# Kernel optimization log

Hardware: AMD Instinct MI355X
Metric: run time of the kernel (lower is better)

Reference implementation:

```python
import jax, jax.numpy as jnp
import numpy as np

B, S, DIN, DIM, H = 2, 2304, 1024, 1024, 16
HEAD_DIM = DIM // H            # 64
ROT_DIM = HEAD_DIM             # partial_rotary_factor = 1
BASE = 10000.0
EPS = 1e-6


def setup_inputs() -> dict:
    key = jax.random.key(0)
    ks = jax.random.split(key, 6)
    return {
        "input": jax.random.normal(ks[0], (B, S, DIN), dtype=jnp.float32),
        "qkv_w": jax.random.normal(ks[1], (3 * DIM, DIN), dtype=jnp.float32) * 0.02,
        "qkv_b": jnp.zeros((3 * DIM,), dtype=jnp.float32),
        "q_scale": jnp.ones((DIM,), dtype=jnp.float32),
        "k_scale": jnp.ones((DIM,), dtype=jnp.float32),
        "proj_w": jax.random.normal(ks[2], (DIN, DIM), dtype=jnp.float32) * 0.02,
        "proj_b": jnp.zeros((DIN,), dtype=jnp.float32),
        "height": 48,
        "width": 48,
    }


def _rms_norm(x, scale):
    # RMSNorm over the full inner dim (QKNorm), learned scale
    var = jnp.mean(x * x, axis=-1, keepdims=True)
    return x * jax.lax.rsqrt(var + EPS) * scale


def _rope_1d(x, pos):
    # x: (b, n, h, d_ax), pos: (n,) float; rotate_half-style RoPE
    d = x.shape[-1]
    inv_freq = 1.0 / (BASE ** (jnp.arange(0, d, 2, dtype=jnp.float32) / d))  # (d/2,)
    ang = pos[:, None] * inv_freq                                            # (n, d/2)
    cos = jnp.concatenate([jnp.cos(ang), jnp.cos(ang)], axis=-1)[None, :, None, :]
    sin = jnp.concatenate([jnp.sin(ang), jnp.sin(ang)], axis=-1)[None, :, None, :]
    x1, x2 = jnp.split(x, 2, axis=-1)
    rot = jnp.concatenate([-x2, x1], axis=-1)
    return x * cos + rot * sin


def _rope_2d(x, height, width):
    # axial 2D RoPE: first half of rotary dims keyed by row, second half by col
    n = height * width
    idx = jnp.arange(n, dtype=jnp.float32)
    rows = jnp.floor(idx / width)
    cols = jnp.mod(idx, width)
    half = ROT_DIM // 2
    x_r = _rope_1d(x[..., :half], rows)
    x_c = _rope_1d(x[..., half:ROT_DIM], cols)
    return jnp.concatenate([x_r, x_c, x[..., ROT_DIM:]], axis=-1)


def reference(input, qkv_w, qkv_b, q_scale, k_scale, proj_w, proj_b, height, width):
    b, n, _ = input.shape
    qkv = input @ qkv_w.T + qkv_b                       # (b, n, 3*dim)
    q, k, v = jnp.split(qkv, 3, axis=-1)
    q = _rms_norm(q, q_scale)
    k = _rms_norm(k, k_scale)
    # (b, n, h, d)
    q = q.reshape(b, n, H, HEAD_DIM)
    k = k.reshape(b, n, H, HEAD_DIM)
    v = v.reshape(b, n, H, HEAD_DIM)
    q = _rope_2d(q, height, width)
    k = _rope_2d(k, height, width)
    scale = HEAD_DIM ** (-0.5)
    # (b, h, q, k)
    scores = jnp.einsum("bqhd,bkhd->bhqk", q, k) * scale
    attn = jax.nn.softmax(scores, axis=-1)
    out = jnp.einsum("bhqk,bkhd->bqhd", attn, v)        # (b, n, h, d)
    out = out.reshape(b, n, DIM)
    return out @ proj_w.T + proj_b
```

## Files before the change

### kernel.cpp

```cpp
#include <hip/hip_runtime.h>
#include <math.h>

#define BB   2
#define SS   2304
#define DINC 1024
#define DIMC 1024
#define HH   16
#define HD   64

typedef _Float16 half_t;
typedef __attribute__((ext_vector_type(4))) _Float16 half4;
typedef __attribute__((ext_vector_type(8))) _Float16 half8;
typedef __attribute__((ext_vector_type(4))) float    f32x4;

#define LOG2E 1.44269504088896340736f
#define EXP2(x) __builtin_amdgcn_exp2f(x)

#define GLOAD_LDS16(gp, lp)                                                     \
    __builtin_amdgcn_global_load_lds(                                           \
        (const __attribute__((address_space(1))) void*)(gp),                    \
        (__attribute__((address_space(3))) void*)(lp), 16, 0, 0)

template<int RB>
__global__ __launch_bounds__(256)
void convert_tile_f16(const float* __restrict__ src, half_t* __restrict__ dst, int K)
{
    constexpr int EPT = RB * 32 / 256;
    const int mb = blockIdx.x;
    const int kb = blockIdx.y;
    const int t  = threadIdx.x;
    const int e0 = t * EPT;
    const int mm = e0 >> 5;
    const int kk = e0 & 31;
    const float* sp = src + (size_t)(mb * RB + mm) * K + kb * 32 + kk;
    half_t*      dp = dst + ((size_t)mb * (K >> 5) + kb) * (RB * 32) + mm * 32 + kk;
    #pragma unroll
    for (int g = 0; g < EPT / 4; ++g) {
        float4 v = *(const float4*)(sp + 4 * g);
        dp[4 * g + 0] = (half_t)v.x; dp[4 * g + 1] = (half_t)v.y;
        dp[4 * g + 2] = (half_t)v.z; dp[4 * g + 3] = (half_t)v.w;
    }
}

template<int BN, bool OUT_HALF>
__global__ __launch_bounds__(256)
void gemm_mfma(const half_t* __restrict__ Ah, const half_t* __restrict__ Bh,
               const float* __restrict__ bias, void* __restrict__ Cout,
               int M, int N, int K)
{
    constexpr int MT = (BN == 128) ? 4 : 2;
    constexpr int NT = 4;
    const int KB = K >> 5;
    __shared__ half_t As[8192];
    __shared__ half_t Bs[2 * BN * 32];

    const int t    = threadIdx.x;
    const int w    = t >> 6;
    const int lane = t & 63;
    const int l15  = lane & 15, quad = lane >> 4;
    const int wr   = (BN == 128) ? (w >> 1) : w;
    const int wc   = (BN == 128) ? (w & 1) : 0;
    const int mb   = blockIdx.y, nb = blockIdx.x;

    f32x4 acc[MT][NT];
    #pragma unroll
    for (int mt = 0; mt < MT; ++mt)
        #pragma unroll
        for (int nt = 0; nt < NT; ++nt) acc[mt][nt] = (f32x4){0.f, 0.f, 0.f, 0.f};

    const half_t* atile = Ah + (size_t)mb * KB * 4096;
    const half_t* btile = Bh + (size_t)nb * KB * (BN * 32);

    for (int kb = 0; kb < KB; kb += 2) {
        #pragma unroll
        for (int u = 0; u < 2; ++u) {
            const half_t* at = atile + (size_t)(kb + u) * 4096;
            const half_t* bt = btile + (size_t)(kb + u) * (BN * 32);
            #pragma unroll
            for (int v = 0; v < 2; ++v) {
                const int ch = w * 2 + v;
                GLOAD_LDS16(at + ch * 512 + lane * 8, As + u * 4096 + ch * 512);
            }
            if (BN == 128) {
                #pragma unroll
                for (int v = 0; v < 2; ++v) {
                    const int ch = w * 2 + v;
                    GLOAD_LDS16(bt + ch * 512 + lane * 8, Bs + u * 4096 + ch * 512);
                }
            } else {
                GLOAD_LDS16(bt + w * 512 + lane * 8, Bs + u * (BN * 32) + w * 512);
            }
        }
        __syncthreads();

        #pragma unroll
        for (int u = 0; u < 2; ++u) {
            half8 af[MT], bf[NT];
            #pragma unroll
            for (int mt = 0; mt < MT; ++mt)
                af[mt] = *(const half8*)(As + u * 4096
                                         + (wr * (MT * 16) + mt * 16 + l15) * 32 + quad * 8);
            #pragma unroll
            for (int nt = 0; nt < NT; ++nt)
                bf[nt] = *(const half8*)(Bs + u * (BN * 32)
                                         + (wc * 64 + nt * 16 + l15) * 32 + quad * 8);
            #pragma unroll
            for (int mt = 0; mt < MT; ++mt)
                #pragma unroll
                for (int nt = 0; nt < NT; ++nt)
                    acc[mt][nt] = __builtin_amdgcn_mfma_f32_16x16x32_f16(
                        af[mt], bf[nt], acc[mt][nt], 0, 0, 0);
        }
        __syncthreads();
    }

    const int bm = mb * 128, bn = nb * BN;
    #pragma unroll
    for (int nt = 0; nt < NT; ++nt) {
        const int n  = bn + wc * 64 + nt * 16 + l15;
        const float bv = bias[n];
        #pragma unroll
        for (int mt = 0; mt < MT; ++mt) {
            const int m0 = bm + wr * (MT * 16) + mt * 16 + quad * 4;
            #pragma unroll
            for (int rg = 0; rg < 4; ++rg) {
                const float v = acc[mt][nt][rg] + bv;
                if (OUT_HALF) ((half_t*)Cout)[(size_t)(m0 + rg) * N + n] = (half_t)v;
                else          ((float*) Cout)[(size_t)(m0 + rg) * N + n] = v;
            }
        }
    }
}

__global__ __launch_bounds__(256)
void normrope_v7(half_t* __restrict__ qkvh, const float* __restrict__ q_scale,
                 const float* __restrict__ k_scale, const int* __restrict__ wptr,
                 half_t* __restrict__ Kf, half_t* __restrict__ Vf)
{
    const int token = blockIdx.x;
    const int s     = token % SS;
    const int b     = token / SS;
    const int w     = *wptr;
    const int t     = threadIdx.x;
    const float rowp = (float)(s / w);
    const float colp = (float)(s % w);

    half_t* base = qkvh + (size_t)token * 3072;

    const int c    = s >> 5;
    const int slot = s & 31;
    const int ktile = (slot >> 2) & 1;
    const int krow  = ((slot >> 3) << 2) + (slot & 3);

    {
        half4 v4 = *(const half4*)(base + 2048 + 4 * t);
        const int dabs0 = 4 * t;
        const int h  = dabs0 >> 6;
        const int sl3 = slot >> 3, sl7 = slot & 7;
        half_t* vdst = Vf + ((size_t)(b * HH + h) * 72 + c) * 2048;
        #pragma unroll
        for (int ii = 0; ii < 4; ++ii) {
            const int d = (dabs0 + ii) & 63;
            vdst[(d >> 4) * 512 + (sl3 * 16 + (d & 15)) * 8 + sl7] = v4[ii];
        }
    }

    __shared__ float buf[DIMC];
    __shared__ float red[4];

    #pragma unroll
    for (int sel = 0; sel < 2; ++sel) {
        half_t* row = base + sel * DIMC;
        const float* scp = sel ? k_scale : q_scale;

        half4 xh = *(const half4*)(row + 4 * t);
        float x0 = (float)xh[0], x1 = (float)xh[1], x2 = (float)xh[2], x3 = (float)xh[3];
        float ss = x0 * x0 + x1 * x1 + x2 * x2 + x3 * x3;
        #pragma unroll
        for (int o = 32; o >= 1; o >>= 1) ss += __shfl_xor(ss, o);
        if ((t & 63) == 0) red[t >> 6] = ss;
        __syncthreads();

        const float rinv = rsqrtf((red[0] + red[1] + red[2] + red[3]) * (1.0f / DIMC) + 1e-6f);
        float4 g = *(const float4*)(scp + 4 * t);
        buf[4 * t + 0] = x0 * rinv * g.x;
        buf[4 * t + 1] = x1 * rinv * g.y;
        buf[4 * t + 2] = x2 * rinv * g.z;
        buf[4 * t + 3] = x3 * rinv * g.w;
        __syncthreads();

        const float qsc = sel ? 1.0f : (0.125f * LOG2E);

        #pragma unroll
        for (int pp = 0; pp < 2; ++pp) {
            const int p = t + pp * 256;
            const int h = p >> 5;
            const int r = p & 31;
            const int j = r & 15;
            const float pos = (r < 16) ? rowp : colp;
            const int d1 = (r < 16) ? j : (32 + j);
            const int d2 = d1 + 16;
            const float freq = exp2f((float)j * -0.83048202372f);
            const float ang  = pos * freq;
            float sn, cs;
            __sincosf(ang, &sn, &cs);
            const float a1 = buf[h * HD + d1], a2 = buf[h * HD + d2];
            const float o1 = (a1 * cs - a2 * sn) * qsc;
            const float o2 = (a2 * cs + a1 * sn) * qsc;
            if (sel == 0) {
                row[h * HD + d1] = (half_t)o1;
                row[h * HD + d2] = (half_t)o2;
            } else {
                half_t* kdst = Kf + ((size_t)(b * HH + h) * 72 + c) * 2048;
                kdst[((ktile << 1) + (d1 >> 5)) * 512
                     + ((((d1 & 31) >> 3) << 4) + krow) * 8 + (d1 & 7)] = (half_t)o1;
                kdst[((ktile << 1) + (d2 >> 5)) * 512
                     + ((((d2 & 31) >> 3) << 4) + krow) * 8 + (d2 & 7)] = (half_t)o2;
            }
        }
        __syncthreads();
    }
}

__global__ __launch_bounds__(256, 3)
void flash_attn_mfma16(const half_t* __restrict__ qkvh, const half_t* __restrict__ Kf,
                       const half_t* __restrict__ Vf, half_t* __restrict__ attn_h)
{
    const int flat = blockIdx.x;
    const int xcd  = flat & 7;
    const int idx  = flat >> 3;
    const int bh   = xcd * 4 + idx / 24;
    const int qtb  = idx % 24;
    const int b    = bh >> 4, h = bh & 15;
    const int t    = threadIdx.x;
    const int w    = t >> 6;
    const int qh   = w >> 1;
    const int jt   = w & 1;
    const int lane = t & 63;
    const int l15  = lane & 15, quad = lane >> 4;

    const size_t tb = (size_t)b * SS;
    const int q0 = qtb * 96;

    __shared__ float mlb[4][48];
    __shared__ float Ob[2][64][49];

    half8 qf[3][2];
    #pragma unroll
    for (int qt = 0; qt < 3; ++qt)
        #pragma unroll
        for (int dg = 0; dg < 2; ++dg)
            qf[qt][dg] = *(const half8*)(qkvh + (tb + q0 + qh * 48 + qt * 16 + l15) * 3072
                                          + h * HD + dg * 32 + quad * 8);

    f32x4 acc[4][3];
    float lacc[3] = {0.f, 0.f, 0.f};
    #pragma unroll
    for (int qt = 0; qt < 3; ++qt)
        #pragma unroll
        for (int dt = 0; dt < 4; ++dt) acc[dt][qt] = (f32x4){0.f, 0.f, 0.f, 0.f};

    const half_t* kpl = Kf + (size_t)bh * 147456 + jt * 2048 + lane * 8;
    const half_t* vpl = Vf + (size_t)bh * 147456 + jt * 2048 + lane * 8;

    half8 k00 = *(const half8*)(kpl);
    half8 k01 = *(const half8*)(kpl + 512);
    half8 k10 = *(const half8*)(kpl + 1024);
    half8 k11 = *(const half8*)(kpl + 1536);
    half8 v0  = *(const half8*)(vpl);
    half8 v1  = *(const half8*)(vpl + 512);
    half8 v2  = *(const half8*)(vpl + 1024);
    half8 v3  = *(const half8*)(vpl + 1536);

    const f32x4 initC = (f32x4){-4.f, -4.f, -4.f, -4.f};

    for (int p = 0; p < 36; ++p) {
        f32x4 scA[3], scB[3];
        __builtin_amdgcn_s_setprio(1);
        #pragma unroll
        for (int qt = 0; qt < 3; ++qt) {
            scA[qt] = initC;
            scA[qt] = __builtin_amdgcn_mfma_f32_16x16x32_f16(k00, qf[qt][0], scA[qt], 0, 0, 0);
            scA[qt] = __builtin_amdgcn_mfma_f32_16x16x32_f16(k01, qf[qt][1], scA[qt], 0, 0, 0);
            scB[qt] = initC;
            scB[qt] = __builtin_amdgcn_mfma_f32_16x16x32_f16(k10, qf[qt][0], scB[qt], 0, 0, 0);
            scB[qt] = __builtin_amdgcn_mfma_f32_16x16x32_f16(k11, qf[qt][1], scB[qt], 0, 0, 0);
        }
        __builtin_amdgcn_s_setprio(0);

        if (p + 1 < 36) {
            const half_t* kN = kpl + (size_t)(p + 1) * 4096;
            k00 = *(const half8*)(kN);
            k01 = *(const half8*)(kN + 512);
            k10 = *(const half8*)(kN + 1024);
            k11 = *(const half8*)(kN + 1536);
        }

        half8 pf[3];
        #pragma unroll
        for (int qt = 0; qt < 3; ++qt) {
            const float a0 = EXP2(scA[qt][0]);
            const float a1 = EXP2(scA[qt][1]);
            const float a2 = EXP2(scA[qt][2]);
            const float a3 = EXP2(scA[qt][3]);
            const float b0 = EXP2(scB[qt][0]);
            const float b1 = EXP2(scB[qt][1]);
            const float b2 = EXP2(scB[qt][2]);
            const float b3 = EXP2(scB[qt][3]);
            lacc[qt] += ((a0 + a1) + (a2 + a3)) + ((b0 + b1) + (b2 + b3));
            pf[qt] = (half8){(half_t)a0, (half_t)a1, (half_t)a2, (half_t)a3,
                             (half_t)b0, (half_t)b1, (half_t)b2, (half_t)b3};
        }

        __builtin_amdgcn_s_setprio(1);
        #pragma unroll
        for (int dt = 0; dt < 4; ++dt) {
            const half8 vf = (dt == 0) ? v0 : (dt == 1) ? v1 : (dt == 2) ? v2 : v3;
            #pragma unroll
            for (int qt = 0; qt < 3; ++qt)
                acc[dt][qt] = __builtin_amdgcn_mfma_f32_16x16x32_f16(
                    vf, pf[qt], acc[dt][qt], 0, 0, 0);
        }
        __builtin_amdgcn_s_setprio(0);

        if (p + 1 < 36) {
            const half_t* vN = vpl + (size_t)(p + 1) * 4096;
            v0 = *(const half8*)(vN);
            v1 = *(const half8*)(vN + 512);
            v2 = *(const half8*)(vN + 1024);
            v3 = *(const half8*)(vN + 1536);
        }
    }

    #pragma unroll
    for (int qt = 0; qt < 3; ++qt) {
        float lq = lacc[qt];
        lq += __shfl_xor(lq, 16);
        lq += __shfl_xor(lq, 32);
        if (quad == 0) mlb[w][qt * 16 + l15] = lq;
    }
    __syncthreads();

    float fac[3];
    #pragma unroll
    for (int qt = 0; qt < 3; ++qt) {
        const int q = qt * 16 + l15;
        fac[qt] = 1.0f / (mlb[qh * 2 + 0][q] + mlb[qh * 2 + 1][q]);
    }

    #pragma unroll
    for (int ph = 0; ph < 2; ++ph) {
        if (jt == ph) {
            #pragma unroll
            for (int dt = 0; dt < 4; ++dt)
                #pragma unroll
                for (int qt = 0; qt < 3; ++qt)
                    #pragma unroll
                    for (int rg = 0; rg < 4; ++rg) {
                        const int d = dt * 16 + quad * 4 + rg;
                        const int q = qt * 16 + l15;
                        const float v = acc[dt][qt][rg] * fac[qt];
                        if (ph == 0) Ob[qh][d][q] = v;
                        else         Ob[qh][d][q] += v;
                    }
        }
        __syncthreads();
    }

    #pragma unroll
    for (int g2 = 0; g2 < 3; ++g2) {
        const int q  = g2 * 32 + (t >> 3);
        const int ds = (t & 7) * 8;
        const int qh2 = (q >= 48) ? 1 : 0;
        const int qq  = q - 48 * qh2;
        const size_t mrow = tb + q0 + q;
        const int mb2 = (int)(mrow >> 7);
        const int mm  = (int)(mrow & 127);
        const int kb2 = (h * HD + ds) >> 5;
        const int kk  = ds & 31;
        half8 o;
        #pragma unroll
        for (int ii = 0; ii < 8; ++ii) o[ii] = (half_t)Ob[qh2][ds + ii][qq];
        *(half8*)(attn_h + ((size_t)mb2 * 32 + kb2) * 4096 + mm * 32 + kk) = o;
    }
}

extern "C" void kernel_launch(void* const* d_in, const int* in_sizes, int n_in,
                              void* d_out, int out_size, void* d_ws, size_t ws_size,
                              hipStream_t stream)
{
    const float* input   = (const float*)d_in[0];
    const float* qkv_w   = (const float*)d_in[1];
    const float* qkv_b   = (const float*)d_in[2];
    const float* q_scale = (const float*)d_in[3];
    const float* k_scale = (const float*)d_in[4];
    const float* proj_w  = (const float*)d_in[5];
    const float* proj_b  = (const float*)d_in[6];
    const int*   width   = (const int*)d_in[8];
    float* out = (float*)d_out;

    half_t* qkvh   = (half_t*)d_ws;
    half_t* attn_h = qkvh   + (size_t)4608 * 3072;
    half_t* Vf     = attn_h + (size_t)4608 * 1024;
    half_t* Ah     = Vf     + (size_t)32 * 72 * 2048;
    half_t* Bh1    = Ah     + (size_t)4608 * 1024;
    half_t* Bh2    = Bh1    + (size_t)3072 * 1024;
    half_t* Kf     = Ah;

    const int M = BB * SS;

    convert_tile_f16<128><<<dim3(M / 128, DINC / 32),        256, 0, stream>>>(input,  Ah,  DINC);
    convert_tile_f16<128><<<dim3(3 * DIMC / 128, DINC / 32), 256, 0, stream>>>(qkv_w, Bh1, DINC);
    convert_tile_f16<64><<<dim3(DINC / 64, DIMC / 32),       256, 0, stream>>>(proj_w, Bh2, DIMC);

    gemm_mfma<128, true><<<dim3(3 * DIMC / 128, M / 128), 256, 0, stream>>>(
        Ah, Bh1, qkv_b, qkvh, M, 3 * DIMC, DINC);

    normrope_v7<<<M, 256, 0, stream>>>(qkvh, q_scale, k_scale, width, Kf, Vf);

    flash_attn_mfma16<<<dim3(768), 256, 0, stream>>>(qkvh, Kf, Vf, attn_h);

    gemm_mfma<64, false><<<dim3(DINC / 64, M / 128), 256, 0, stream>>>(
        attn_h, Bh2, proj_b, out, M, DINC, DIMC);
}
```

Baseline: 240.3 us.

## Use 192x96 tiles for the QKV GEMM so the grid fills one occupancy wave

Adds a dedicated QKV projection GEMM kernel with 192x96 block tiles and a 6x3 MFMA fragment grid per wave. The grid becomes 768 blocks, which with a minimum of 3 blocks per CU fits the device in one wave. It also changes the fp32-to-fp16 tile conversion so consecutive threads read consecutive float4s, for better coalescing, and matches its tiling to the new A and B tile shapes. The trade-off is higher register pressure from 18 accumulators per wave, and the new tile is specialised to fixed sizes.

Result: faster. 231.0 us (-3.9%).

```diff
diff --git a/kernel.cpp b/kernel.cpp
--- a/kernel.cpp
+++ b/kernel.cpp
@@ -25,20 +25,91 @@
 __global__ __launch_bounds__(256)
 void convert_tile_f16(const float* __restrict__ src, half_t* __restrict__ dst, int K)
 {
-    constexpr int EPT = RB * 32 / 256;
+    constexpr int NG = RB * 32 / 1024;
     const int mb = blockIdx.x;
     const int kb = blockIdx.y;
     const int t  = threadIdx.x;
-    const int e0 = t * EPT;
-    const int mm = e0 >> 5;
-    const int kk = e0 & 31;
-    const float* sp = src + (size_t)(mb * RB + mm) * K + kb * 32 + kk;
-    half_t*      dp = dst + ((size_t)mb * (K >> 5) + kb) * (RB * 32) + mm * 32 + kk;
-    #pragma unroll
-    for (int g = 0; g < EPT / 4; ++g) {
-        float4 v = *(const float4*)(sp + 4 * g);
-        dp[4 * g + 0] = (half_t)v.x; dp[4 * g + 1] = (half_t)v.y;
-        dp[4 * g + 2] = (half_t)v.z; dp[4 * g + 3] = (half_t)v.w;
+    const float* sp0 = src + (size_t)mb * RB * K + kb * 32;
+    half_t*      dp0 = dst + ((size_t)mb * (K >> 5) + kb) * (RB * 32);
+    #pragma unroll
+    for (int g = 0; g < NG; ++g) {
+        const int e  = g * 1024 + t * 4;
+        const int mm = e >> 5, kk = e & 31;
+        float4 v = *(const float4*)(sp0 + (size_t)mm * K + kk);
+        dp0[e + 0] = (half_t)v.x; dp0[e + 1] = (half_t)v.y;
+        dp0[e + 2] = (half_t)v.z; dp0[e + 3] = (half_t)v.w;
+    }
+}
+
+__global__ __launch_bounds__(256, 3)
+void gemm_mfma192(const half_t* __restrict__ Ah, const half_t* __restrict__ Bh,
+                  const float* __restrict__ bias, half_t* __restrict__ Cout)
+{
+    const int t    = threadIdx.x;
+    const int w    = t >> 6;
+    const int lane = t & 63;
+    const int l15  = lane & 15, quad = lane >> 4;
+    const int wr   = w >> 1;
+    const int wc   = w & 1;
+    const int mb   = blockIdx.y;
+    const int nb   = blockIdx.x;
+
+    __shared__ __align__(16) half_t As[2][6144];
+    __shared__ __align__(16) half_t Bs[2][3072];
+
+    f32x4 acc[6][3];
+    #pragma unroll
+    for (int mt = 0; mt < 6; ++mt)
+        #pragma unroll
+        for (int nt = 0; nt < 3; ++nt) acc[mt][nt] = (f32x4){0.f, 0.f, 0.f, 0.f};
+
+    const half_t* atile = Ah + (size_t)mb * 32 * 6144;
+    const half_t* btile = Bh + (size_t)nb * 32 * 3072;
+
+    for (int kb = 0; kb < 32; kb += 2) {
+        #pragma unroll
+        for (int u = 0; u < 2; ++u) {
+            const half_t* at = atile + (size_t)(kb + u) * 6144;
+            const half_t* bt = btile + (size_t)(kb + u) * 3072;
+            for (int ch = w; ch < 18; ch += 4) {
+                if (ch < 12) GLOAD_LDS16(at + ch * 512 + lane * 8, &As[u][ch * 512]);
+                else         GLOAD_LDS16(bt + (ch - 12) * 512 + lane * 8,
+                                         &Bs[u][(ch - 12) * 512]);
+            }
+        }
+        __syncthreads();
+
+        #pragma unroll
+        for (int u = 0; u < 2; ++u) {
+            half8 af[6], bf[3];
+            #pragma unroll
+            for (int mt = 0; mt < 6; ++mt)
+                af[mt] = *(const half8*)(&As[u][(wr * 96 + mt * 16 + l15) * 32 + quad * 8]);
+            #pragma unroll
+            for (int nt = 0; nt < 3; ++nt)
+                bf[nt] = *(const half8*)(&Bs[u][(wc * 48 + nt * 16 + l15) * 32 + quad * 8]);
+            #pragma unroll
+            for (int mt = 0; mt < 6; ++mt)
+                #pragma unroll
+                for (int nt = 0; nt < 3; ++nt)
+                    acc[mt][nt] = __builtin_amdgcn_mfma_f32_16x16x32_f16(
+                        af[mt], bf[nt], acc[mt][nt], 0, 0, 0);
+        }
+        __syncthreads();
+    }
+
+    const int bm = mb * 192, bn = nb * 96;
+    #pragma unroll
+    for (int nt = 0; nt < 3; ++nt) {
+        const int n  = bn + wc * 48 + nt * 16 + l15;
+        const float bv = bias[n];
+        #pragma unroll
+        for (int mt = 0; mt < 6; ++mt) {
+            const int m0 = bm + wr * 96 + mt * 16 + quad * 4;
+            #pragma unroll
+            for (int rg = 0; rg < 4; ++rg)
+                Cout[(size_t)(m0 + rg) * 3072 + n] = (half_t)(acc[mt][nt][rg] + bv);
+        }
     }
 }
 
@@ -81,15 +152,7 @@
                 const int ch = w * 2 + v;
                 GLOAD_LDS16(at + ch * 512 + lane * 8, As + u * 4096 + ch * 512);
             }
-            if (BN == 128) {
-                #pragma unroll
-                for (int v = 0; v < 2; ++v) {
-                    const int ch = w * 2 + v;
-                    GLOAD_LDS16(bt + ch * 512 + lane * 8, Bs + u * 4096 + ch * 512);
-                }
-            } else {
-                GLOAD_LDS16(bt + w * 512 + lane * 8, Bs + u * (BN * 32) + w * 512);
-            }
+            GLOAD_LDS16(bt + w * 512 + lane * 8, Bs + u * (BN * 32) + w * 512);
         }
         __syncthreads();
 
@@ -409,12 +472,12 @@
 
     const int M = BB * SS;
 
-    convert_tile_f16<128><<<dim3(M / 128, DINC / 32),        256, 0, stream>>>(input,  Ah,  DINC);
-    convert_tile_f16<128><<<dim3(3 * DIMC / 128, DINC / 32), 256, 0, stream>>>(qkv_w, Bh1, DINC);
+    convert_tile_f16<192><<<dim3(M / 192, DINC / 32),        256, 0, stream>>>(input,  Ah,  DINC);
+    convert_tile_f16<96><<<dim3(3 * DIMC / 96, DINC / 32),   256, 0, stream>>>(qkv_w, Bh1, DINC);
     convert_tile_f16<64><<<dim3(DINC / 64, DIMC / 32),       256, 0, stream>>>(proj_w, Bh2, DIMC);
 
-    gemm_mfma<128, true><<<dim3(3 * DIMC / 128, M / 128), 256, 0, stream>>>(
-        Ah, Bh1, qkv_b, qkvh, M, 3 * DIMC, DINC);
+    gemm_mfma192<<<dim3(3 * DIMC / 96, M / 192), 256, 0, stream>>>(
+        Ah, Bh1, qkv_b, qkvh);
 
     normrope_v7<<<M, 256, 0, stream>>>(qkvh, q_scale, k_scale, width, Kf, Vf);
 
```
